# Kernel optimization log

Measured on AMD Instinct MI355X. Metric: run time of the kernel, lower is better.

The kernel has to match this reference:

```python
import jax, jax.numpy as jnp
import numpy as np

EMBED_DIM = 768
NUM_HEADS = 12
FF_DIM = 3072
HEAD_DIM = EMBED_DIM // NUM_HEADS
LN_EPS = 1e-5


def setup_inputs() -> dict:
    key = jax.random.key(0)
    ks = jax.random.split(key, 10)
    C, F = EMBED_DIM, FF_DIM
    s = lambda d: 1.0 / np.sqrt(d)
    return {
        "x": jax.random.normal(ks[0], (2, 2048, C), dtype=jnp.float32),
        "w_qkv": jax.random.normal(ks[1], (C, 3 * C), dtype=jnp.float32) * s(C),
        "w_out": jax.random.normal(ks[2], (C, C), dtype=jnp.float32) * s(C),
        "ln1_g": jnp.ones((C,), jnp.float32),
        "ln1_b": jnp.zeros((C,), jnp.float32),
        "ln2_g": jnp.ones((C,), jnp.float32),
        "ln2_b": jnp.zeros((C,), jnp.float32),
        "w1": jax.random.normal(ks[3], (C, F), dtype=jnp.float32) * s(C),
        "b1": jnp.zeros((F,), jnp.float32),
        "w2": jax.random.normal(ks[4], (F, C), dtype=jnp.float32) * s(F),
        "b2": jnp.zeros((C,), jnp.float32),
    }


def _layernorm(x, g, b):
    mu = jnp.mean(x, axis=-1, keepdims=True)
    var = jnp.var(x, axis=-1, keepdims=True)
    return (x - mu) * jax.lax.rsqrt(var + LN_EPS) * g + b


def _attention(x, w_qkv, w_out):
    B, T, C = x.shape
    qkv = x @ w_qkv                               # [B,T,3C]
    q, k, v = jnp.split(qkv, 3, axis=2)
    def heads(t):  # [B,T,C] -> [B,H,T,Dh]
        return t.reshape(B, T, NUM_HEADS, HEAD_DIM).transpose(0, 2, 1, 3)
    q, k, v = heads(q), heads(k), heads(v)
    att = jnp.einsum("bhqd,bhkd->bhqk", q, k) / np.sqrt(HEAD_DIM)
    mask = jnp.tril(jnp.ones((T, T), bool))
    att = jnp.where(mask, att, -jnp.inf)
    att = jax.nn.softmax(att, axis=-1)
    out = jnp.einsum("bhqk,bhkd->bhqd", att, v)   # [B,H,T,Dh]
    out = out.transpose(0, 2, 1, 3).reshape(B, T, C)
    return out @ w_out


def reference(x, w_qkv, w_out, ln1_g, ln1_b, ln2_g, ln2_b, w1, b1, w2, b2):
    x = x + _attention(_layernorm(x, ln1_g, ln1_b), w_qkv, w_out)
    h = _layernorm(x, ln2_g, ln2_b)
    h = jax.nn.gelu(h @ w1 + b1, approximate=False) @ w2 + b2
    return x + h
```

## Files before the change

kernel.cpp:

```cpp
#include <hip/hip_runtime.h>
#include <hip/hip_bf16.h>
#include <math.h>

typedef __attribute__((ext_vector_type(8))) short short8;
typedef __attribute__((ext_vector_type(4))) float f32x4;
typedef __attribute__((address_space(1))) const void CG;
typedef __attribute__((address_space(3))) void LS;

#define LOAD_LDS16(src, dst) __builtin_amdgcn_global_load_lds((CG*)(src), (LS*)(dst), 16, 0, 0)

__device__ __forceinline__ short f2bf(float f) {
  union { float f; unsigned u; } v; v.f = f;
  unsigned r = v.u + 0x7fffu + ((v.u >> 16) & 1u);
  return (short)(r >> 16);
}

__global__ __launch_bounds__(256) void transp_all(const float* __restrict__ w_qkv,
                                                  const float* __restrict__ w_out,
                                                  const float* __restrict__ w1,
                                                  const float* __restrict__ w2,
                                                  short* __restrict__ wqkvT,
                                                  short* __restrict__ woutT,
                                                  short* __restrict__ w1T,
                                                  short* __restrict__ w2T) {
  __shared__ short t[32][33];
  int bid = blockIdx.x;
  const float* W; short* Wt; int K, N, nx, id;
  if (bid < 1728)      { W = w_qkv; Wt = wqkvT; K = 768;  N = 2304; nx = 72; id = bid; }
  else if (bid < 2304) { W = w_out; Wt = woutT; K = 768;  N = 768;  nx = 24; id = bid - 1728; }
  else if (bid < 4608) { W = w1;    Wt = w1T;   K = 768;  N = 3072; nx = 96; id = bid - 2304; }
  else                 { W = w2;    Wt = w2T;   K = 3072; N = 768;  nx = 24; id = bid - 4608; }
  int n0 = (id % nx) << 5, k0 = (id / nx) << 5;
  int tid = threadIdx.x;
#pragma unroll
  for (int p = 0; p < 4; ++p) {
    int e = tid + (p << 8);
    int r = e >> 5, c = e & 31;
    t[r][c] = f2bf(W[(size_t)(k0 + r) * N + n0 + c]);
  }
  __syncthreads();
#pragma unroll
  for (int p = 0; p < 4; ++p) {
    int e = tid + (p << 8);
    int r = e >> 5, c = e & 31;
    Wt[(size_t)(n0 + r) * K + k0 + c] = t[c][r];
  }
}

__global__ __launch_bounds__(256) void ln_kernel(const float* __restrict__ x,
                                                 const float* __restrict__ g,
                                                 const float* __restrict__ b,
                                                 short* __restrict__ out) {
  int row = blockIdx.x;
  const float* xr = x + (size_t)row * 768;
  int tid = threadIdx.x;
  float v0 = xr[tid], v1 = xr[tid + 256], v2 = xr[tid + 512];
  float s = v0 + v1 + v2;
  float ss = v0 * v0 + v1 * v1 + v2 * v2;
#pragma unroll
  for (int m = 1; m < 64; m <<= 1) { s += __shfl_xor(s, m); ss += __shfl_xor(ss, m); }
  __shared__ float red[8];
  int w = tid >> 6;
  if ((tid & 63) == 0) { red[w] = s; red[w + 4] = ss; }
  __syncthreads();
  s = red[0] + red[1] + red[2] + red[3];
  ss = red[4] + red[5] + red[6] + red[7];
  float mean = s * (1.0f / 768.0f);
  float var = ss * (1.0f / 768.0f) - mean * mean;
  float rs = rsqrtf(var + 1e-5f);
  short* outr = out + (size_t)row * 768;
  outr[tid]       = f2bf((v0 - mean) * rs * g[tid]       + b[tid]);
  outr[tid + 256] = f2bf((v1 - mean) * rs * g[tid + 256] + b[tid + 256]);
  outr[tid + 512] = f2bf((v2 - mean) * rs * g[tid + 512] + b[tid + 512]);
}

template <int EPI>
__global__ __launch_bounds__(512, 2) void gemm256(
    const short* __restrict__ A, const short* __restrict__ Bt,
    int M, int N, int K,
    short* __restrict__ outQ, short* __restrict__ outK, short* __restrict__ outVt,
    float* __restrict__ outF, short* __restrict__ outB,
    const float* __restrict__ bias, const float* __restrict__ resid) {
  __shared__ short lA[2][256 * 64];
  __shared__ short lB[2][256 * 64];
  int tid = threadIdx.x;
  int lane = tid & 63, w = tid >> 6;
  int li = lane & 15, g = lane >> 4;
  int wr = w >> 2, wc = w & 3;

  int nx = gridDim.x, ny = gridDim.y;
  int nwg = nx * ny;
  int fid = (int)blockIdx.y * nx + (int)blockIdx.x;
  int nid = (fid & 7) * (nwg >> 3) + (fid >> 3);
  const int GM = 8;
  int npg = GM * nx;
  int grp = nid / npg;
  int fm = grp * GM;
  int gs = min(GM, ny - fm);
  int lid = nid - grp * npg;
  int bm = (fm + lid % gs) << 8;
  int bn = (lid / gs) << 8;

  size_t lda = (EPI == 4) ? 3072 : (size_t)K;
  int koff = (EPI == 4) ? (int)blockIdx.z * 768 : 0;

  int r8 = lane >> 3, cph = lane & 7;
  int csrc = cph ^ r8;
  const short* asA[4];
  const short* bsB[4];
#pragma unroll
  for (int p = 0; p < 4; ++p) {
    int row = p * 64 + w * 8 + r8;
    asA[p] = A + (size_t)(bm + row) * lda + koff + csrc * 8;
    bsB[p] = Bt + (size_t)(bn + row) * lda + koff + csrc * 8;
  }

#define STG(buf, ki)                                                      \
  do {                                                                    \
    int kk = (ki) << 6;                                                   \
    LOAD_LDS16(asA[0] + kk, (char*)lA[buf] + (w << 10));                  \
    LOAD_LDS16(asA[1] + kk, (char*)lA[buf] + 8192 + (w << 10));           \
    LOAD_LDS16(asA[2] + kk, (char*)lA[buf] + 16384 + (w << 10));          \
    LOAD_LDS16(asA[3] + kk, (char*)lA[buf] + 24576 + (w << 10));          \
    LOAD_LDS16(bsB[0] + kk, (char*)lB[buf] + (w << 10));                  \
    LOAD_LDS16(bsB[1] + kk, (char*)lB[buf] + 8192 + (w << 10));           \
    LOAD_LDS16(bsB[2] + kk, (char*)lB[buf] + 16384 + (w << 10));          \
    LOAD_LDS16(bsB[3] + kk, (char*)lB[buf] + 24576 + (w << 10));          \
  } while (0)

  f32x4 zero = {0.f, 0.f, 0.f, 0.f};
  f32x4 acc[8][4];
#pragma unroll
  for (int i = 0; i < 8; ++i)
#pragma unroll
    for (int j = 0; j < 4; ++j) acc[i][j] = zero;

  int nk = K >> 6;
  STG(0, 0);
  for (int ki = 0; ki < nk; ++ki) {
    int cur = ki & 1;
    __syncthreads();
    if (ki + 1 < nk) STG(cur ^ 1, ki + 1);
    const short* Ac = lA[cur];
    const short* Bc = lB[cur];
#pragma unroll
    for (int kc = 0; kc < 2; ++kc) {
      int ch = (((kc << 2) | g) ^ (li & 7)) << 3;
      short8 bf[4];
#pragma unroll
      for (int ct = 0; ct < 4; ++ct)
        bf[ct] = *(const short8*)&Bc[(wc * 64 + ct * 16 + li) * 64 + ch];
#pragma unroll
      for (int rt = 0; rt < 8; ++rt) {
        short8 af = *(const short8*)&Ac[(wr * 128 + rt * 16 + li) * 64 + ch];
#pragma unroll
        for (int ct = 0; ct < 4; ++ct)
          acc[rt][ct] = __builtin_amdgcn_mfma_f32_16x16x32_bf16(af, bf[ct], acc[rt][ct], 0, 0, 0);
      }
    }
  }
#undef STG

#pragma unroll
  for (int rt = 0; rt < 8; ++rt) {
    int mbase = bm + wr * 128 + rt * 16 + g * 4;
#pragma unroll
    for (int ct = 0; ct < 4; ++ct) {
      int n = bn + wc * 64 + ct * 16 + li;
      f32x4 c = acc[rt][ct];
      if (EPI == 0) {
        if (n < 768) {
          int h = n >> 6, d = n & 63;
#pragma unroll
          for (int i = 0; i < 4; ++i) {
            int tok = mbase + i;
            int bb = tok >> 11, t = tok & 2047;
            outQ[((size_t)((bb * 12 + h) * 2048 + t) << 6) + d] = f2bf(c[i]);
          }
        } else if (n < 1536) {
          int nn = n - 768;
          int h = nn >> 6, d = nn & 63;
#pragma unroll
          for (int i = 0; i < 4; ++i) {
            int tok = mbase + i;
            int bb = tok >> 11, t = tok & 2047;
            outK[((size_t)((bb * 12 + h) * 2048 + t) << 6) + d] = f2bf(c[i]);
          }
        } else {
          int nn = n - 1536;
          int h = nn >> 6, d = nn & 63;
          int bb = mbase >> 11, t = mbase & 2047;
          ushort4 pk;
          pk.x = (unsigned short)f2bf(c[0]);
          pk.y = (unsigned short)f2bf(c[1]);
          pk.z = (unsigned short)f2bf(c[2]);
          pk.w = (unsigned short)f2bf(c[3]);
          *(ushort4*)((unsigned short*)outVt + (((size_t)((bb * 12 + h) * 64 + d)) << 11) + t) = pk;
        }
      } else if (EPI == 2) {
        float bv = bias[n];
#pragma unroll
        for (int i = 0; i < 4; ++i) {
          int m = mbase + i;
          float xx = c[i] + bv;
          float gel = 0.5f * xx * (1.0f + erff(xx * 0.70710678118654752f));
          outB[(size_t)m * N + n] = f2bf(gel);
        }
      } else {
        bool last = (blockIdx.z == 3);
        float bv = last ? bias[n] : 0.f;
#pragma unroll
        for (int i = 0; i < 4; ++i) {
          int m = mbase + i;
          float add = c[i] + bv + (last ? resid[(size_t)m * N + n] : 0.f);
          atomicAdd(&outF[(size_t)m * N + n], add);
        }
      }
    }
  }
}

template <int EPI>
__global__ __launch_bounds__(256, 3) void gemm_bt(
    const short* __restrict__ A, const short* __restrict__ Bt,
    int M, int N, int K,
    float* __restrict__ outF, const float* __restrict__ resid) {
  __shared__ short lA[3][128 * 32];
  __shared__ short lB[3][128 * 32];
  int tid = threadIdx.x;
  int lane = tid & 63, w = tid >> 6;
  int li = lane & 15, g = lane >> 4;

  int nx = gridDim.x, ny = gridDim.y;
  int nwg = nx * ny;
  int fid = (int)blockIdx.y * nx + (int)blockIdx.x;
  int nid = (fid & 7) * (nwg >> 3) + (fid >> 3);
  const int GM = 8;
  int npg = GM * nx;
  int grp = nid / npg;
  int fm = grp * GM;
  int gs = min(GM, ny - fm);
  int lid = nid - grp * npg;
  int bm = (fm + lid % gs) << 7;
  int bn = (lid / gs) << 7;

  int wrow = (w >> 1) << 6, wcol = (w & 1) << 6;

  const short* as[2];
  const short* bs[2];
#pragma unroll
  for (int p = 0; p < 2; ++p) {
    int v = tid + (p << 8);
    int row = v >> 2;
    int lc = (v & 3) ^ ((row ^ (row >> 2)) & 3);
    as[p] = A + (size_t)(bm + row) * K + lc * 8;
    bs[p] = Bt + (size_t)(bn + row) * K + lc * 8;
  }
  int sg = (g ^ ((li ^ (li >> 2)) & 3)) << 3;

  f32x4 zero = {0.f, 0.f, 0.f, 0.f};
  f32x4 acc[4][4];
#pragma unroll
  for (int i = 0; i < 4; ++i)
#pragma unroll
    for (int j = 0; j < 4; ++j) acc[i][j] = zero;

#define GSTAGE(buf, ki)                                                 \
  do {                                                                  \
    int kk = (ki) << 5;                                                 \
    LOAD_LDS16(as[0] + kk, (char*)lA[buf] + (w << 10));                 \
    LOAD_LDS16(as[1] + kk, (char*)lA[buf] + 4096 + (w << 10));          \
    LOAD_LDS16(bs[0] + kk, (char*)lB[buf] + (w << 10));                 \
    LOAD_LDS16(bs[1] + kk, (char*)lB[buf] + 4096 + (w << 10));          \
  } while (0)

  auto compute = [&](int bufidx) {
    const short* lAc = lA[bufidx];
    const short* lBc = lB[bufidx];
    short8 af[4], bf[4];
#pragma unroll
    for (int rt = 0; rt < 4; ++rt)
      af[rt] = *(const short8*)&lAc[(wrow + rt * 16 + li) * 32 + sg];
#pragma unroll
    for (int ct = 0; ct < 4; ++ct)
      bf[ct] = *(const short8*)&lBc[(wcol + ct * 16 + li) * 32 + sg];
#pragma unroll
    for (int rt = 0; rt < 4; ++rt)
#pragma unroll
      for (int ct = 0; ct < 4; ++ct)
        acc[rt][ct] = __builtin_amdgcn_mfma_f32_16x16x32_bf16(af[rt], bf[ct], acc[rt][ct], 0, 0, 0);
  };

  int nk = K >> 5;
  GSTAGE(0, 0);
  GSTAGE(1, 1);
  int cur = 0, n1 = 1, n2 = 2;
  for (int ki = 0; ki < nk - 1; ++ki) {
    asm volatile("s_waitcnt vmcnt(4)" ::: "memory");
    __builtin_amdgcn_s_barrier();
    __builtin_amdgcn_sched_barrier(0);
    if (ki + 2 < nk) GSTAGE(n2, ki + 2);
    compute(cur);
    int t = cur; cur = n1; n1 = n2; n2 = t;
  }
  asm volatile("s_waitcnt vmcnt(0)" ::: "memory");
  __builtin_amdgcn_s_barrier();
  __builtin_amdgcn_sched_barrier(0);
  compute(cur);
#undef GSTAGE

#pragma unroll
  for (int rt = 0; rt < 4; ++rt) {
    int mbase = bm + wrow + rt * 16 + g * 4;
#pragma unroll
    for (int ct = 0; ct < 4; ++ct) {
      int n = bn + wcol + ct * 16 + li;
      f32x4 c = acc[rt][ct];
#pragma unroll
      for (int i = 0; i < 4; ++i) {
        int m = mbase + i;
        outF[(size_t)m * N + n] = c[i] + resid[(size_t)m * N + n];
      }
    }
  }
}

__global__ __launch_bounds__(256, 3) void attn_kernel(const short* __restrict__ Q,
                                                      const short* __restrict__ Kk,
                                                      const short* __restrict__ Vt,
                                                      unsigned short* __restrict__ o_part,
                                                      float* __restrict__ ml_part) {
  __shared__ short lK[2][64 * 64];
  __shared__ short lV[2][64 * 64];
  __shared__ short lP[4][32 * 64];
  int tid = threadIdx.x;
  int lane = tid & 63, w = tid >> 6;
  int li = lane & 15, g = lane >> 4;
  int bh = blockIdx.y;
  int cid = 39 - (int)blockIdx.x;
  int qt = 0, cum = 0;
  while (true) { int n = (qt >> 2) + 1; if (cid < cum + n) break; cum += n; ++qt; }
  int c = cid - cum;
  int nch = (qt >> 2) + 1;
  int nt = (qt + 1) << 1;
  int bq = nt / nch, rem = nt % nch;
  int t0 = c * bq + (c < rem ? c : rem);
  int t1 = t0 + bq + (c < rem ? 1 : 0);

  int qbase = (qt << 7) + (w << 5);
  const short* Qb = Q + ((size_t)bh << 17);
  const short* Kb = Kk + ((size_t)bh << 17);
  const short* Vb = Vt + ((size_t)bh << 17);

  short8 qf[2][2];
#pragma unroll
  for (int rt = 0; rt < 2; ++rt)
#pragma unroll
    for (int kc = 0; kc < 2; ++kc)
      qf[rt][kc] = *(const short8*)&Qb[(size_t)(qbase + rt * 16 + li) * 64 + kc * 32 + g * 8];

  int r0 = tid >> 3, s0 = (tid & 7) ^ (r0 & 7);
  int r1 = r0 + 32,  s1 = (tid & 7) ^ (r1 & 7);
  const short* kS0 = Kb + r0 * 64 + s0 * 8;
  const short* kS1 = Kb + r1 * 64 + s1 * 8;
  const short* vS0 = Vb + (size_t)r0 * 2048 + s0 * 8;
  const short* vS1 = Vb + (size_t)r1 * 2048 + s1 * 8;

#define STAGE(buf, kt)                                                        \
  do {                                                                        \
    LOAD_LDS16(kS0 + (size_t)(kt) * 4096, (char*)lK[buf] + (w << 10));        \
    LOAD_LDS16(kS1 + (size_t)(kt) * 4096, (char*)lK[buf] + 4096 + (w << 10)); \
    LOAD_LDS16(vS0 + (size_t)(kt) * 64,   (char*)lV[buf] + (w << 10));        \
    LOAD_LDS16(vS1 + (size_t)(kt) * 64,   (char*)lV[buf] + 4096 + (w << 10)); \
  } while (0)

  const short8 kOnes = {0x3F80, 0x3F80, 0x3F80, 0x3F80, 0x3F80, 0x3F80, 0x3F80, 0x3F80};
  f32x4 zero = {0.f, 0.f, 0.f, 0.f};
  f32x4 o[2][4];
  f32x4 lrow[2];
  float mrow[2] = {-1e30f, -1e30f};
#pragma unroll
  for (int rt = 0; rt < 2; ++rt) {
    lrow[rt] = zero;
#pragma unroll
    for (int ct = 0; ct < 4; ++ct) o[rt][ct] = zero;
  }

  int diagKt = qbase >> 6;
  const float SCALE = 0.18033688011112042f;
  int sw = li & 7;
  unsigned short* Pw = (unsigned short*)lP[w];

  STAGE(0, t0);

  for (int kt = t0; kt < t1; ++kt) {
    int cur = (kt - t0) & 1;
    __syncthreads();
    if (kt + 1 < t1) STAGE(cur ^ 1, kt + 1);

    if (kt <= diagKt) {
      const short* Kc = lK[cur];
      const short* Vc = lV[cur];

      f32x4 s[2][4];
#pragma unroll
      for (int rt = 0; rt < 2; ++rt)
#pragma unroll
        for (int ct = 0; ct < 4; ++ct) s[rt][ct] = zero;
#pragma unroll
      for (int kc = 0; kc < 2; ++kc)
#pragma unroll
        for (int ct = 0; ct < 4; ++ct) {
          short8 kf = *(const short8*)&Kc[(ct * 16 + li) * 64 + ((((kc << 2) | g) ^ sw) << 3)];
#pragma unroll
          for (int rt = 0; rt < 2; ++rt)
            s[rt][ct] = __builtin_amdgcn_mfma_f32_16x16x32_bf16(qf[rt][kc], kf, s[rt][ct], 0, 0, 0);
        }

      if (kt == diagKt) {
        int kb0 = kt << 6;
#pragma unroll
        for (int rt = 0; rt < 2; ++rt) {
          int qrow0 = qbase + rt * 16 + g * 4;
#pragma unroll
          for (int ct = 0; ct < 4; ++ct) {
            int kcol = kb0 + ct * 16 + li;
#pragma unroll
            for (int i = 0; i < 4; ++i)
              if (kcol > qrow0 + i) s[rt][ct][i] = -1e30f;
          }
        }
      }

#pragma unroll
      for (int rt = 0; rt < 2; ++rt) {
        float tm = s[rt][0][0];
#pragma unroll
        for (int ct = 0; ct < 4; ++ct)
#pragma unroll
          for (int i = 0; i < 4; ++i) tm = fmaxf(tm, s[rt][ct][i]);
#pragma unroll
        for (int m2 = 1; m2 < 64; m2 <<= 1) tm = fmaxf(tm, __shfl_xor(tm, m2));
        if (tm > mrow[rt] + 8.0f) {
          float corr = exp2f((mrow[rt] - tm) * SCALE);
          mrow[rt] = tm;
#pragma unroll
          for (int i = 0; i < 4; ++i) lrow[rt][i] *= corr;
#pragma unroll
          for (int ct = 0; ct < 4; ++ct)
#pragma unroll
            for (int i = 0; i < 4; ++i) o[rt][ct][i] *= corr;
        }
#pragma unroll
        for (int ct = 0; ct < 4; ++ct)
#pragma unroll
          for (int i = 0; i < 4; ++i) {
            float p = exp2f((s[rt][ct][i] - mrow[rt]) * SCALE);
            int row = rt * 16 + (g << 2) + i;
            int col = (ct << 4) + li;
            int ch = (col >> 3) ^ (row & 7);
            Pw[(row << 6) + (ch << 3) + (col & 7)] = (unsigned short)f2bf(p);
          }
      }

      f32x4 psum[2];
      psum[0] = zero; psum[1] = zero;
#pragma unroll
      for (int kc = 0; kc < 2; ++kc) {
        short8 vf[4];
#pragma unroll
        for (int ct = 0; ct < 4; ++ct)
          vf[ct] = *(const short8*)&Vc[(ct * 16 + li) * 64 + ((((kc << 2) | g) ^ sw) << 3)];
#pragma unroll
        for (int rt = 0; rt < 2; ++rt) {
          short8 pf = *(const short8*)&lP[w][(rt * 16 + li) * 64 + ((((kc << 2) | g) ^ sw) << 3)];
#pragma unroll
          for (int ct = 0; ct < 4; ++ct)
            o[rt][ct] = __builtin_amdgcn_mfma_f32_16x16x32_bf16(pf, vf[ct], o[rt][ct], 0, 0, 0);
          psum[rt] = __builtin_amdgcn_mfma_f32_16x16x32_bf16(pf, kOnes, psum[rt], 0, 0, 0);
        }
      }
#pragma unroll
      for (int rt = 0; rt < 2; ++rt)
#pragma unroll
        for (int i = 0; i < 4; ++i) lrow[rt][i] += psum[rt][i];
    }
  }
#undef STAGE

  int pid = bh * 40 + cid;
#pragma unroll
  for (int rt = 0; rt < 2; ++rt)
#pragma unroll
    for (int ct = 0; ct < 4; ++ct) {
      int col = (ct << 4) + li;
      int row0 = (w << 5) + (rt << 4) + (g << 2);
      ushort4 pk;
      pk.x = (unsigned short)f2bf(o[rt][ct][0]);
      pk.y = (unsigned short)f2bf(o[rt][ct][1]);
      pk.z = (unsigned short)f2bf(o[rt][ct][2]);
      pk.w = (unsigned short)f2bf(o[rt][ct][3]);
      *(ushort4*)&o_part[((size_t)pid * 64 + col) * 128 + row0] = pk;
    }
  if (li == 0) {
    float2* mlp = (float2*)ml_part;
#pragma unroll
    for (int rt = 0; rt < 2; ++rt)
#pragma unroll
      for (int i = 0; i < 4; ++i) {
        int row = (w << 5) + (rt << 4) + (g << 2) + i;
        mlp[(size_t)pid * 128 + row] = make_float2(mrow[rt], lrow[rt][i]);
      }
  }
}

__global__ __launch_bounds__(256) void attn_combine(const unsigned short* __restrict__ o_part,
                                                    const float* __restrict__ ml_part,
                                                    short* __restrict__ O) {
  __shared__ float wgt[4][128];
  int qt = blockIdx.x, bh = blockIdx.y;
  int a = qt >> 2, bb = qt & 3;
  int c0 = 2 * a * (a - 1) + a * bb + qt;
  int nch = a + 1;
  int pid0 = bh * 40 + c0;
  int tid = threadIdx.x;
  const float SCALE = 0.18033688011112042f;
  const float2* mlp = (const float2*)ml_part;

  if (tid < 128) {
    int row = tid;
    float mv[4] = {-1e30f, -1e30f, -1e30f, -1e30f};
    float lv[4] = {0.f, 0.f, 0.f, 0.f};
#pragma unroll
    for (int c = 0; c < 4; ++c)
      if (c < nch) {
        float2 ml = mlp[(size_t)(pid0 + c) * 128 + row];
        mv[c] = ml.x; lv[c] = ml.y;
      }
    float M = fmaxf(fmaxf(mv[0], mv[1]), fmaxf(mv[2], mv[3]));
    float u[4];
    float L = 0.f;
#pragma unroll
    for (int c = 0; c < 4; ++c) {
      u[c] = (c < nch) ? exp2f((mv[c] - M) * SCALE) : 0.f;
      L += lv[c] * u[c];
    }
    float inv = 1.0f / L;
#pragma unroll
    for (int c = 0; c < 4; ++c) wgt[c][row] = u[c] * inv;
  }
  __syncthreads();

  int col = tid & 63, rg = tid >> 6;
  int b = bh / 12, h = bh % 12;
  size_t obase[4];
#pragma unroll
  for (int c = 0; c < 4; ++c) obase[c] = ((size_t)(pid0 + c) * 64 + col) * 128;
  for (int r = 0; r < 32; ++r) {
    int row = (rg << 5) + r;
    float acc = 0.f;
#pragma unroll
    for (int c = 0; c < 4; ++c)
      if (c < nch) {
        union { unsigned u; float f; } cv;
        cv.u = ((unsigned)o_part[obase[c] + row]) << 16;
        acc += cv.f * wgt[c][row];
      }
    int t = (qt << 7) + row;
    O[((size_t)(b * 2048 + t)) * 768 + h * 64 + col] = f2bf(acc);
  }
}

extern "C" void kernel_launch(void* const* d_in, const int* in_sizes, int n_in,
                              void* d_out, int out_size, void* d_ws, size_t ws_size,
                              hipStream_t stream) {
  const float* x     = (const float*)d_in[0];
  const float* w_qkv = (const float*)d_in[1];
  const float* w_out = (const float*)d_in[2];
  const float* ln1g  = (const float*)d_in[3];
  const float* ln1b  = (const float*)d_in[4];
  const float* ln2g  = (const float*)d_in[5];
  const float* ln2b  = (const float*)d_in[6];
  const float* w1    = (const float*)d_in[7];
  const float* b1    = (const float*)d_in[8];
  const float* w2    = (const float*)d_in[9];
  const float* b2    = (const float*)d_in[10];
  float* out = (float*)d_out;
  char* ws = (char*)d_ws;

  short* wqkvT = (short*)(ws + 0);
  short* woutT = (short*)(ws + 3538944);
  short* w1T   = (short*)(ws + 4718592);
  short* w2T   = (short*)(ws + 9437184);
  short* qb    = (short*)(ws + 14155776);
  short* kb    = (short*)(ws + 20447232);
  short* vtb   = (short*)(ws + 26738688);
  short* attnb = (short*)(ws + 33030144);
  short* ab    = qb;
  short* xnb   = (short*)(ws + 39321600);
  float* x2b   = (float*)(ws + 45613056);
  unsigned short* o_part = (unsigned short*)(ws + 39321600);
  float* ml_part = (float*)(ws + 55050240);

  transp_all<<<dim3(6912), 256, 0, stream>>>(w_qkv, w_out, w1, w2, wqkvT, woutT, w1T, w2T);

  ln_kernel<<<dim3(4096), 256, 0, stream>>>(x, ln1g, ln1b, xnb);

  gemm256<0><<<dim3(9, 16), 512, 0, stream>>>(xnb, wqkvT, 4096, 2304, 768,
                                              qb, kb, vtb, nullptr, nullptr, nullptr, nullptr);

  attn_kernel<<<dim3(40, 24), 256, 0, stream>>>(qb, kb, vtb, o_part, ml_part);
  attn_combine<<<dim3(16, 24), 256, 0, stream>>>(o_part, ml_part, attnb);

  gemm_bt<1><<<dim3(6, 32), 256, 0, stream>>>(attnb, woutT, 4096, 768, 768, x2b, x);

  ln_kernel<<<dim3(4096), 256, 0, stream>>>(x2b, ln2g, ln2b, xnb);

  gemm256<2><<<dim3(12, 16), 512, 0, stream>>>(xnb, w1T, 4096, 3072, 768,
                                               nullptr, nullptr, nullptr, nullptr, ab, b1, nullptr);

  hipMemsetAsync(out, 0, (size_t)4096 * 768 * 4, stream);
  gemm256<4><<<dim3(3, 16, 4), 512, 0, stream>>>(ab, w2T, 4096, 768, 768,
                                                 nullptr, nullptr, nullptr, out, nullptr, b2, x2b);
}
```

Baseline: 284.4 us.

## Interleave split global-to-LDS staging with quadrant MFMA blocks in GEMM main loop

Restructures the GEMM K-loop so each tile's compute runs in four quadrant MFMA phases, with the next tile's global-to-LDS loads issued in four quarters between them. It uses explicit waitcnt and s_barrier handling in place of __syncthreads, plus s_setprio and sched_barrier to fix instruction order. The aim is to hide load latency behind matrix work and cut LDS fragment register pressure. In exchange the waitcnt counts become fragile and the scheduler loses freedom to reorder.

```diff
diff --git a/kernel.cpp b/kernel.cpp
--- a/kernel.cpp
+++ b/kernel.cpp
@@ -115,17 +115,15 @@
     bsB[p] = Bt + (size_t)(bn + row) * lda + koff + csrc * 8;
   }
 
-#define STG(buf, ki)                                                      \
-  do {                                                                    \
-    int kk = (ki) << 6;                                                   \
-    LOAD_LDS16(asA[0] + kk, (char*)lA[buf] + (w << 10));                  \
-    LOAD_LDS16(asA[1] + kk, (char*)lA[buf] + 8192 + (w << 10));           \
-    LOAD_LDS16(asA[2] + kk, (char*)lA[buf] + 16384 + (w << 10));          \
-    LOAD_LDS16(asA[3] + kk, (char*)lA[buf] + 24576 + (w << 10));          \
-    LOAD_LDS16(bsB[0] + kk, (char*)lB[buf] + (w << 10));                  \
-    LOAD_LDS16(bsB[1] + kk, (char*)lB[buf] + 8192 + (w << 10));           \
-    LOAD_LDS16(bsB[2] + kk, (char*)lB[buf] + 16384 + (w << 10));          \
-    LOAD_LDS16(bsB[3] + kk, (char*)lB[buf] + 24576 + (w << 10));          \
+#define STGH(buf, h, kk)                                                       \
+  do {                                                                         \
+    if ((h) < 2) {                                                             \
+      LOAD_LDS16(asA[(h)*2] + (kk), (char*)lA[buf] + (h)*16384 + (w << 10));   \
+      LOAD_LDS16(asA[(h)*2+1] + (kk), (char*)lA[buf] + (h)*16384 + 8192 + (w << 10)); \
+    } else {                                                                   \
+      LOAD_LDS16(bsB[((h)-2)*2] + (kk), (char*)lB[buf] + ((h)-2)*16384 + (w << 10)); \
+      LOAD_LDS16(bsB[((h)-2)*2+1] + (kk), (char*)lB[buf] + ((h)-2)*16384 + 8192 + (w << 10)); \
+    }                                                                          \
   } while (0)
 
   f32x4 zero = {0.f, 0.f, 0.f, 0.f};
@@ -135,31 +133,106 @@
 #pragma unroll
     for (int j = 0; j < 4; ++j) acc[i][j] = zero;
 
-  int nk = K >> 6;
-  STG(0, 0);
-  for (int ki = 0; ki < nk; ++ki) {
-    int cur = ki & 1;
-    __syncthreads();
-    if (ki + 1 < nk) STG(cur ^ 1, ki + 1);
+  int rowA0 = wr * 128;
+  int colB0 = wc * 64;
+  int sw7 = li & 7;
+
+  auto compute_tile = [&](int cur, int nxt, int kk1, bool stg) {
     const short* Ac = lA[cur];
     const short* Bc = lB[cur];
-#pragma unroll
-    for (int kc = 0; kc < 2; ++kc) {
-      int ch = (((kc << 2) | g) ^ (li & 7)) << 3;
-      short8 bf[4];
-#pragma unroll
-      for (int ct = 0; ct < 4; ++ct)
-        bf[ct] = *(const short8*)&Bc[(wc * 64 + ct * 16 + li) * 64 + ch];
-#pragma unroll
-      for (int rt = 0; rt < 8; ++rt) {
-        short8 af = *(const short8*)&Ac[(wr * 128 + rt * 16 + li) * 64 + ch];
-#pragma unroll
-        for (int ct = 0; ct < 4; ++ct)
-          acc[rt][ct] = __builtin_amdgcn_mfma_f32_16x16x32_bf16(af, bf[ct], acc[rt][ct], 0, 0, 0);
-      }
-    }
-  }
-#undef STG
+    short8 afr[4][2], bfr[2][2], bfr2[2][2];
+#pragma unroll
+    for (int ct = 0; ct < 2; ++ct)
+#pragma unroll
+      for (int kc = 0; kc < 2; ++kc)
+        bfr[ct][kc] = *(const short8*)&Bc[(colB0 + ct * 16 + li) * 64 + ((((kc << 2) | g) ^ sw7) << 3)];
+#pragma unroll
+    for (int rt = 0; rt < 4; ++rt)
+#pragma unroll
+      for (int kc = 0; kc < 2; ++kc)
+        afr[rt][kc] = *(const short8*)&Ac[(rowA0 + rt * 16 + li) * 64 + ((((kc << 2) | g) ^ sw7) << 3)];
+    __builtin_amdgcn_s_setprio(1);
+#pragma unroll
+    for (int rt = 0; rt < 4; ++rt)
+#pragma unroll
+      for (int ct = 0; ct < 2; ++ct)
+#pragma unroll
+        for (int kc = 0; kc < 2; ++kc)
+          acc[rt][ct] = __builtin_amdgcn_mfma_f32_16x16x32_bf16(afr[rt][kc], bfr[ct][kc], acc[rt][ct], 0, 0, 0);
+    __builtin_amdgcn_s_setprio(0);
+    __builtin_amdgcn_sched_barrier(0);
+    if (stg) STGH(nxt, 1, kk1);
+    __builtin_amdgcn_sched_barrier(0);
+#pragma unroll
+    for (int ct = 0; ct < 2; ++ct)
+#pragma unroll
+      for (int kc = 0; kc < 2; ++kc)
+        bfr2[ct][kc] = *(const short8*)&Bc[(colB0 + (ct + 2) * 16 + li) * 64 + ((((kc << 2) | g) ^ sw7) << 3)];
+    __builtin_amdgcn_s_setprio(1);
+#pragma unroll
+    for (int rt = 0; rt < 4; ++rt)
+#pragma unroll
+      for (int ct = 0; ct < 2; ++ct)
+#pragma unroll
+        for (int kc = 0; kc < 2; ++kc)
+          acc[rt][ct + 2] = __builtin_amdgcn_mfma_f32_16x16x32_bf16(afr[rt][kc], bfr2[ct][kc], acc[rt][ct + 2], 0, 0, 0);
+    __builtin_amdgcn_s_setprio(0);
+    __builtin_amdgcn_sched_barrier(0);
+    if (stg) STGH(nxt, 2, kk1);
+    __builtin_amdgcn_sched_barrier(0);
+#pragma unroll
+    for (int rt = 0; rt < 4; ++rt)
+#pragma unroll
+      for (int kc = 0; kc < 2; ++kc)
+        afr[rt][kc] = *(const short8*)&Ac[(rowA0 + (rt + 4) * 16 + li) * 64 + ((((kc << 2) | g) ^ sw7) << 3)];
+    __builtin_amdgcn_s_setprio(1);
+#pragma unroll
+    for (int rt = 0; rt < 4; ++rt)
+#pragma unroll
+      for (int ct = 0; ct < 2; ++ct)
+#pragma unroll
+        for (int kc = 0; kc < 2; ++kc)
+          acc[rt + 4][ct + 2] = __builtin_amdgcn_mfma_f32_16x16x32_bf16(afr[rt][kc], bfr2[ct][kc], acc[rt + 4][ct + 2], 0, 0, 0);
+    __builtin_amdgcn_s_setprio(0);
+    __builtin_amdgcn_sched_barrier(0);
+    if (stg) STGH(nxt, 3, kk1);
+    __builtin_amdgcn_sched_barrier(0);
+    __builtin_amdgcn_s_setprio(1);
+#pragma unroll
+    for (int rt = 0; rt < 4; ++rt)
+#pragma unroll
+      for (int ct = 0; ct < 2; ++ct)
+#pragma unroll
+        for (int kc = 0; kc < 2; ++kc)
+          acc[rt + 4][ct] = __builtin_amdgcn_mfma_f32_16x16x32_bf16(afr[rt][kc], bfr[ct][kc], acc[rt + 4][ct], 0, 0, 0);
+    __builtin_amdgcn_s_setprio(0);
+    __builtin_amdgcn_sched_barrier(0);
+  };
+
+  int nk = K >> 6;
+  STGH(0, 0, 0); STGH(0, 1, 0); STGH(0, 2, 0); STGH(0, 3, 0);
+  for (int t = 0; t < nk - 1; ++t) {
+    int cur = t & 1, nxt = cur ^ 1;
+    int kk1 = (t + 1) << 6;
+    asm volatile("s_waitcnt lgkmcnt(0)" ::: "memory");
+    __builtin_amdgcn_s_barrier();
+    __builtin_amdgcn_sched_barrier(0);
+    STGH(nxt, 0, kk1);
+    asm volatile("s_waitcnt vmcnt(2)" ::: "memory");
+    __builtin_amdgcn_s_barrier();
+    __builtin_amdgcn_sched_barrier(0);
+    compute_tile(cur, nxt, kk1, true);
+  }
+  {
+    int cur = (nk - 1) & 1;
+    asm volatile("s_waitcnt lgkmcnt(0)" ::: "memory");
+    __builtin_amdgcn_s_barrier();
+    asm volatile("s_waitcnt vmcnt(0)" ::: "memory");
+    __builtin_amdgcn_s_barrier();
+    __builtin_amdgcn_sched_barrier(0);
+    compute_tile(cur, 0, 0, false);
+  }
+#undef STGH
 
 #pragma unroll
   for (int rt = 0; rt < 8; ++rt) {
```

New measurement: 275.7 us. 1.03x faster.
